# Kernel tuning notes

Hardware: AMD Instinct MI355X
Metric: run time of the kernel (lower is better)

The kernel has to match this reference:

```python
import jax, jax.numpy as jnp
import numpy as np

N_QUBITS = 8


def setup_inputs() -> dict:
    key = jax.random.key(0)
    ks = jax.random.split(key, 6)
    B, S, E, F = 8, 4096, 1024, 4096
    return {
        "x": jax.random.normal(ks[0], (B, S, E), dtype=jnp.float32),
        "theta": jax.random.normal(ks[1], (N_QUBITS,), dtype=jnp.float32),
        "w1": jax.random.normal(ks[2], (F, N_QUBITS), dtype=jnp.float32) * 0.1,
        "b1": jax.random.normal(ks[3], (F,), dtype=jnp.float32) * 0.02,
        "w2": jax.random.normal(ks[4], (E, F), dtype=jnp.float32) * 0.02,
        "b2": jax.random.normal(ks[5], (E,), dtype=jnp.float32) * 0.02,
    }


def reference(x, theta, w1, b1, w2, b2):
    # Quantum layer: per wire i, |0> -RX(x_i)-> -RY(theta_i)-> measure <Z>.
    # No entangling gates => state factorizes; <Z_i> = cos(x_i) * cos(theta_i).
    q = jnp.cos(x[..., :N_QUBITS]) * jnp.cos(theta)  # [B, S, n_qubits]
    h = jax.nn.relu(jnp.einsum("bsq,fq->bsf", q, w1) + b1)  # [B, S, ffn_dim]
    return jnp.einsum("bsf,ef->bse", h, w2) + b2  # [B, S, embed_dim]
```

## Files before the change

kernel.cpp:

```cpp
#include <hip/hip_runtime.h>
#include <stdint.h>

typedef unsigned short u16;
typedef __attribute__((ext_vector_type(8))) short short8v;
typedef __attribute__((ext_vector_type(4))) float float4v;

static __device__ __forceinline__ u16 f2bf(float f) {
    union { float f; uint32_t u; } v; v.f = f;
    uint32_t u = v.u;
    uint32_t r = (u + 0x7fffu + ((u >> 16) & 1u)) >> 16;
    return (u16)r;
}

__global__ __launch_bounds__(256) void w2cvt_kernel(const float* __restrict__ w2,
                                                    u16* __restrict__ W) {
    size_t i = ((size_t)blockIdx.x * 256 + threadIdx.x) * 4;
    float4 v = *(const float4*)&w2[i];
    ushort4 o;
    o.x = f2bf(v.x); o.y = f2bf(v.y); o.z = f2bf(v.z); o.w = f2bf(v.w);
    *(ushort4*)&W[i] = o;
}

__global__ __launch_bounds__(256) void h_kernel(const float* __restrict__ x,
                                                const float* __restrict__ theta,
                                                const float* __restrict__ w1,
                                                const float* __restrict__ b1,
                                                u16* __restrict__ H, int m0) {
    constexpr int ROWS = 16;
    __shared__ float qs[ROWS][8];
    const int tid = threadIdx.x;
    const int r0 = blockIdx.x * ROWS;
    if (tid < ROWS * 8) {
        int r = tid >> 3, i = tid & 7;
        qs[r][i] = cosf(x[(size_t)(m0 + r0 + r) * 1024 + i]) * cosf(theta[i]);
    }
    __syncthreads();
    for (int qi = 0; qi < 4; ++qi) {
        const int f4 = (qi * 256 + tid) * 4;
        float4 wa[4], wb[4];
        float bb[4];
#pragma unroll
        for (int c = 0; c < 4; ++c) {
            wa[c] = *(const float4*)&w1[(size_t)(f4 + c) * 8];
            wb[c] = *(const float4*)&w1[(size_t)(f4 + c) * 8 + 4];
            bb[c] = b1[f4 + c];
        }
        for (int r = 0; r < ROWS; ++r) {
            float qv[8];
#pragma unroll
            for (int i = 0; i < 8; ++i) qv[i] = qs[r][i];
            ushort4 hv;
#pragma unroll
            for (int c = 0; c < 4; ++c) {
                float a = bb[c];
                a += qv[0] * wa[c].x + qv[1] * wa[c].y + qv[2] * wa[c].z + qv[3] * wa[c].w;
                a += qv[4] * wb[c].x + qv[5] * wb[c].y + qv[6] * wb[c].z + qv[7] * wb[c].w;
                a = fmaxf(a, 0.f);
                ((u16*)&hv)[c] = f2bf(a);
            }
            *(ushort4*)&H[(size_t)(r0 + r) * 4096 + f4] = hv;
        }
    }
}

__global__ __launch_bounds__(256) void gemm_kernel(const u16* __restrict__ A,
                                                   const u16* __restrict__ B,
                                                   const float* __restrict__ b2,
                                                   float* __restrict__ C) {
    constexpr int K = 4096, N = 1024;
    constexpr int BM = 128, BK = 64;
    constexpr int NKS = K / BK;
    __shared__ __align__(16) u16 lds[2 * 8192];

    const int tid = threadIdx.x;
    const int wv = tid >> 6, lane = tid & 63;
    const int bn = blockIdx.x & 7, bm = blockIdx.x >> 3;

    auto stage = [&](int ks) {
#pragma unroll
        for (int i = 0; i < 4; ++i) {
            const int sp = wv * 4 + i;
            const int li = sp * 64 + lane;
            const int row = li >> 3;
            const int j = li & 7;
            const int koff = 8 * (j ^ (row & 7));
            const u16* srcA = A + (size_t)(bm * BM + row) * K + ks * BK + koff;
            __builtin_amdgcn_global_load_lds(
                (const __attribute__((address_space(1))) void*)srcA,
                (__attribute__((address_space(3))) void*)&lds[sp * 512], 16, 0, 0);
            const u16* srcB = B + (size_t)(bn * BM + row) * K + ks * BK + koff;
            __builtin_amdgcn_global_load_lds(
                (const __attribute__((address_space(1))) void*)srcB,
                (__attribute__((address_space(3))) void*)&lds[8192 + sp * 512], 16, 0, 0);
        }
    };

    float4v acc[4][4];
#pragma unroll
    for (int mi = 0; mi < 4; ++mi)
#pragma unroll
        for (int ni = 0; ni < 4; ++ni)
            acc[mi][ni] = (float4v){0.f, 0.f, 0.f, 0.f};

    const int wm = (wv & 1) * 64, wn = (wv >> 1) * 64;
    const int lr = lane & 15, kg = lane >> 4;

    stage(0);
    for (int ks = 0; ks < NKS; ++ks) {
        __syncthreads();
#pragma unroll
        for (int kk = 0; kk < 2; ++kk) {
            short8v av[4], bv[4];
#pragma unroll
            for (int mi = 0; mi < 4; ++mi) {
                const int row = wm + mi * 16 + lr;
                const int byteoff = row * 128 + ((kk * 64 + kg * 16) ^ ((row & 7) << 4));
                av[mi] = *(const short8v*)((const char*)lds + byteoff);
            }
#pragma unroll
            for (int ni = 0; ni < 4; ++ni) {
                const int row = wn + ni * 16 + lr;
                const int byteoff = 16384 + row * 128 + ((kk * 64 + kg * 16) ^ ((row & 7) << 4));
                bv[ni] = *(const short8v*)((const char*)lds + byteoff);
            }
#pragma unroll
            for (int mi = 0; mi < 4; ++mi)
#pragma unroll
                for (int ni = 0; ni < 4; ++ni)
                    acc[mi][ni] = __builtin_amdgcn_mfma_f32_16x16x32_bf16(
                        av[mi], bv[ni], acc[mi][ni], 0, 0, 0);
        }
        __syncthreads();
        if (ks + 1 < NKS) stage(ks + 1);
    }

    float b2v[4];
#pragma unroll
    for (int ni = 0; ni < 4; ++ni) b2v[ni] = b2[bn * BM + wn + ni * 16 + lr];
#pragma unroll
    for (int mi = 0; mi < 4; ++mi)
#pragma unroll
        for (int ni = 0; ni < 4; ++ni) {
            const int col = bn * BM + wn + ni * 16 + lr;
#pragma unroll
            for (int j = 0; j < 4; ++j) {
                const int row = bm * BM + wm + mi * 16 + kg * 4 + j;
                C[(size_t)row * N + col] = acc[mi][ni][j] + b2v[ni];
            }
        }
}

__global__ __launch_bounds__(256) void naive_kernel(const float* __restrict__ x,
                                                    const float* __restrict__ theta,
                                                    const float* __restrict__ w1,
                                                    const float* __restrict__ b1,
                                                    const float* __restrict__ w2,
                                                    const float* __restrict__ b2,
                                                    float* __restrict__ out) {
    const int m = blockIdx.x;
    __shared__ float h[4096];
    __shared__ float q[8];
    if (threadIdx.x < 8)
        q[threadIdx.x] = cosf(x[(size_t)m * 1024 + threadIdx.x]) * cosf(theta[threadIdx.x]);
    __syncthreads();
    for (int f = threadIdx.x; f < 4096; f += 256) {
        float a = b1[f];
#pragma unroll
        for (int i = 0; i < 8; ++i) a += q[i] * w1[(size_t)f * 8 + i];
        h[f] = fmaxf(a, 0.f);
    }
    __syncthreads();
    for (int e = threadIdx.x; e < 1024; e += 256) {
        float a = b2[e];
        const float* wr = w2 + (size_t)e * 4096;
        for (int f = 0; f < 4096; ++f) a += h[f] * wr[f];
        out[(size_t)m * 1024 + e] = a;
    }
}

extern "C" void kernel_launch(void* const* d_in, const int* in_sizes, int n_in,
                              void* d_out, int out_size, void* d_ws, size_t ws_size,
                              hipStream_t stream) {
    const float* x     = (const float*)d_in[0];
    const float* theta = (const float*)d_in[1];
    const float* w1    = (const float*)d_in[2];
    const float* b1    = (const float*)d_in[3];
    const float* w2    = (const float*)d_in[4];
    const float* b2    = (const float*)d_in[5];
    float* out = (float*)d_out;

    const int M = 32768, K = 4096, N = 1024;
    const size_t w2b_bytes = (size_t)N * K * 2;

    size_t avail = ws_size > w2b_bytes ? ws_size - w2b_bytes : 0;
    long long mc_ll = (long long)(avail / ((size_t)K * 2));
    int Mc = (int)((mc_ll > 32768) ? 32768 : mc_ll);
    Mc = (Mc / 128) * 128;
    if (Mc > 8192) Mc = 8192;

    if (Mc < 128) {
        naive_kernel<<<dim3(M), dim3(256), 0, stream>>>(x, theta, w1, b1, w2, b2, out);
        return;
    }

    u16* w2b = (u16*)d_ws;
    u16* Hb  = (u16*)((char*)d_ws + w2b_bytes);

    w2cvt_kernel<<<dim3((N * K) / 1024), dim3(256), 0, stream>>>(w2, w2b);

    for (int m0 = 0; m0 < M; m0 += Mc) {
        const int rows = (M - m0 < Mc) ? (M - m0) : Mc;
        h_kernel<<<dim3(rows / 16), dim3(256), 0, stream>>>(x, theta, w1, b1, Hb, m0);
        gemm_kernel<<<dim3((rows / 128) * 8), dim3(256), 0, stream>>>(
            Hb, w2b, b2, out + (size_t)m0 * N);
    }
}
```

Measured before the change: 585.3 us.

## Rework GEMM into 256x128 tile with triple-buffered LDS pipeline and 8 waves

The GEMM moves from 128x128 tiles with 4 waves and a single-stage load to 256x128 tiles with 8 waves. Global-to-LDS loads are triple-buffered two tiles ahead and split across the two k-halves, with explicit vmcnt waits, barriers and setprio around the MFMA blocks, so memory latency overlaps compute. Block indices are remapped so neighbouring blocks share A rows for better L2 reuse. The h_kernel now has each thread write 8 bf16 outputs per row over 32 rows. The cost is larger LDS use (144KB per block) and fragile hand-tuned waitcnt logic.

```diff
diff --git a/kernel.cpp b/kernel.cpp
--- a/kernel.cpp
+++ b/kernel.cpp
@@ -26,74 +26,86 @@
                                                 const float* __restrict__ w1,
                                                 const float* __restrict__ b1,
                                                 u16* __restrict__ H, int m0) {
-    constexpr int ROWS = 16;
-    __shared__ float qs[ROWS][8];
+    __shared__ float qs[32][8];
     const int tid = threadIdx.x;
-    const int r0 = blockIdx.x * ROWS;
-    if (tid < ROWS * 8) {
+    const int rb = blockIdx.x >> 1;
+    const int fb = blockIdx.x & 1;
+    const int r0 = rb * 32;
+    {
         int r = tid >> 3, i = tid & 7;
         qs[r][i] = cosf(x[(size_t)(m0 + r0 + r) * 1024 + i]) * cosf(theta[i]);
     }
     __syncthreads();
-    for (int qi = 0; qi < 4; ++qi) {
-        const int f4 = (qi * 256 + tid) * 4;
-        float4 wa[4], wb[4];
-        float bb[4];
-#pragma unroll
-        for (int c = 0; c < 4; ++c) {
-            wa[c] = *(const float4*)&w1[(size_t)(f4 + c) * 8];
-            wb[c] = *(const float4*)&w1[(size_t)(f4 + c) * 8 + 4];
-            bb[c] = b1[f4 + c];
-        }
-        for (int r = 0; r < ROWS; ++r) {
-            float qv[8];
-#pragma unroll
-            for (int i = 0; i < 8; ++i) qv[i] = qs[r][i];
-            ushort4 hv;
-#pragma unroll
-            for (int c = 0; c < 4; ++c) {
-                float a = bb[c];
-                a += qv[0] * wa[c].x + qv[1] * wa[c].y + qv[2] * wa[c].z + qv[3] * wa[c].w;
-                a += qv[4] * wb[c].x + qv[5] * wb[c].y + qv[6] * wb[c].z + qv[7] * wb[c].w;
-                a = fmaxf(a, 0.f);
-                ((u16*)&hv)[c] = f2bf(a);
-            }
-            *(ushort4*)&H[(size_t)(r0 + r) * 4096 + f4] = hv;
-        }
-    }
-}
-
-__global__ __launch_bounds__(256) void gemm_kernel(const u16* __restrict__ A,
-                                                   const u16* __restrict__ B,
-                                                   const float* __restrict__ b2,
-                                                   float* __restrict__ C) {
+    const int f8 = (fb * 256 + tid) * 8;
+    float4 w[16];
+    float bb[8];
+#pragma unroll
+    for (int c = 0; c < 8; ++c) {
+        w[2 * c]     = *(const float4*)&w1[(size_t)(f8 + c) * 8];
+        w[2 * c + 1] = *(const float4*)&w1[(size_t)(f8 + c) * 8 + 4];
+        bb[c] = b1[f8 + c];
+    }
+    for (int r = 0; r < 32; ++r) {
+        float qv[8];
+#pragma unroll
+        for (int i = 0; i < 8; ++i) qv[i] = qs[r][i];
+        short8v hv;
+#pragma unroll
+        for (int c = 0; c < 8; ++c) {
+            float a = bb[c];
+            a += qv[0] * w[2*c].x + qv[1] * w[2*c].y + qv[2] * w[2*c].z + qv[3] * w[2*c].w;
+            a += qv[4] * w[2*c+1].x + qv[5] * w[2*c+1].y + qv[6] * w[2*c+1].z + qv[7] * w[2*c+1].w;
+            a = fmaxf(a, 0.f);
+            hv[c] = (short)f2bf(a);
+        }
+        *(short8v*)&H[(size_t)(r0 + r) * 4096 + f8] = hv;
+    }
+}
+
+__global__ __launch_bounds__(512, 2) void gemm_kernel(const u16* __restrict__ A,
+                                                      const u16* __restrict__ B,
+                                                      const float* __restrict__ b2,
+                                                      float* __restrict__ C, int nbm) {
     constexpr int K = 4096, N = 1024;
-    constexpr int BM = 128, BK = 64;
-    constexpr int NKS = K / BK;
-    __shared__ __align__(16) u16 lds[2 * 8192];
+    constexpr int NKT = K / 64;
+    __shared__ __align__(16) u16 lds[3 * 24576];
 
     const int tid = threadIdx.x;
     const int wv = tid >> 6, lane = tid & 63;
-    const int bn = blockIdx.x & 7, bm = blockIdx.x >> 3;
-
-    auto stage = [&](int ks) {
-#pragma unroll
-        for (int i = 0; i < 4; ++i) {
-            const int sp = wv * 4 + i;
-            const int li = sp * 64 + lane;
-            const int row = li >> 3;
-            const int j = li & 7;
-            const int koff = 8 * (j ^ (row & 7));
-            const u16* srcA = A + (size_t)(bm * BM + row) * K + ks * BK + koff;
-            __builtin_amdgcn_global_load_lds(
-                (const __attribute__((address_space(1))) void*)srcA,
-                (__attribute__((address_space(3))) void*)&lds[sp * 512], 16, 0, 0);
-            const u16* srcB = B + (size_t)(bn * BM + row) * K + ks * BK + koff;
-            __builtin_amdgcn_global_load_lds(
-                (const __attribute__((address_space(1))) void*)srcB,
-                (__attribute__((address_space(3))) void*)&lds[8192 + sp * 512], 16, 0, 0);
-        }
-    };
+
+    const int qq = nbm;
+    const int bid = (int)blockIdx.x;
+    const int lbid = (bid & 7) * qq + (bid >> 3);
+    const int bm = lbid >> 3, bn = lbid & 7;
+
+    const u16* Ab = A + (size_t)bm * 256 * K;
+    const u16* Bb = B + (size_t)bn * 128 * K;
+
+    const u16* srcA[4]; int dstA[4];
+#pragma unroll
+    for (int u = 0; u < 4; ++u) {
+        const int idx = u * 512 + tid;
+        const int row = idx >> 3, j = idx & 7;
+        srcA[u] = Ab + (size_t)row * K + 8 * (j ^ (row & 7));
+        dstA[u] = idx * 8;
+    }
+    const u16* srcB[2]; int dstB[2];
+#pragma unroll
+    for (int u = 0; u < 2; ++u) {
+        const int idx = u * 512 + tid;
+        const int row = idx >> 3, j = idx & 7;
+        srcB[u] = Bb + (size_t)row * K + 8 * (j ^ (row & 7));
+        dstB[u] = 16384 + idx * 8;
+    }
+
+#define STAGE_A(kt, bufbase, u)                                               \
+    __builtin_amdgcn_global_load_lds(                                         \
+        (const __attribute__((address_space(1))) void*)(srcA[u] + (kt) * 64), \
+        (__attribute__((address_space(3))) void*)((bufbase) + dstA[u]), 16, 0, 0)
+#define STAGE_B(kt, bufbase, u)                                               \
+    __builtin_amdgcn_global_load_lds(                                         \
+        (const __attribute__((address_space(1))) void*)(srcB[u] + (kt) * 64), \
+        (__attribute__((address_space(3))) void*)((bufbase) + dstB[u]), 16, 0, 0)
 
     float4v acc[4][4];
 #pragma unroll
@@ -102,49 +114,91 @@
         for (int ni = 0; ni < 4; ++ni)
             acc[mi][ni] = (float4v){0.f, 0.f, 0.f, 0.f};
 
-    const int wm = (wv & 1) * 64, wn = (wv >> 1) * 64;
+    const int wm = (wv >> 1) * 64, wn = (wv & 1) * 64;
     const int lr = lane & 15, kg = lane >> 4;
 
-    stage(0);
-    for (int ks = 0; ks < NKS; ++ks) {
-        __syncthreads();
-#pragma unroll
-        for (int kk = 0; kk < 2; ++kk) {
-            short8v av[4], bv[4];
-#pragma unroll
-            for (int mi = 0; mi < 4; ++mi) {
-                const int row = wm + mi * 16 + lr;
-                const int byteoff = row * 128 + ((kk * 64 + kg * 16) ^ ((row & 7) << 4));
-                av[mi] = *(const short8v*)((const char*)lds + byteoff);
-            }
-#pragma unroll
-            for (int ni = 0; ni < 4; ++ni) {
-                const int row = wn + ni * 16 + lr;
-                const int byteoff = 16384 + row * 128 + ((kk * 64 + kg * 16) ^ ((row & 7) << 4));
-                bv[ni] = *(const short8v*)((const char*)lds + byteoff);
-            }
-#pragma unroll
-            for (int mi = 0; mi < 4; ++mi)
-#pragma unroll
-                for (int ni = 0; ni < 4; ++ni)
-                    acc[mi][ni] = __builtin_amdgcn_mfma_f32_16x16x32_bf16(
-                        av[mi], bv[ni], acc[mi][ni], 0, 0, 0);
-        }
-        __syncthreads();
-        if (ks + 1 < NKS) stage(ks + 1);
-    }
+    {
+        u16* b0 = &lds[0];
+        u16* b1b = &lds[24576];
+        STAGE_A(0, b0, 0); STAGE_A(0, b0, 1); STAGE_A(0, b0, 2); STAGE_A(0, b0, 3);
+        STAGE_B(0, b0, 0); STAGE_B(0, b0, 1);
+        STAGE_A(1, b1b, 0); STAGE_A(1, b1b, 1); STAGE_A(1, b1b, 2); STAGE_A(1, b1b, 3);
+        STAGE_B(1, b1b, 0); STAGE_B(1, b1b, 1);
+    }
+    asm volatile("s_waitcnt vmcnt(6)" ::: "memory");
+    __builtin_amdgcn_s_barrier();
+
+    int bi = 0, si = 2;
+    for (int kt = 0; kt < NKT; ++kt) {
+        char* buf = (char*)&lds[bi * 24576];
+        u16* sbuf = &lds[si * 24576];
+        const bool doStage = (kt + 2 < NKT);
+
+        if (doStage) { STAGE_A(kt + 2, sbuf, 0); STAGE_A(kt + 2, sbuf, 1); STAGE_A(kt + 2, sbuf, 2); }
+        short8v av0[4], bv0[4];
+#pragma unroll
+        for (int mi = 0; mi < 4; ++mi) {
+            const int row = wm + mi * 16 + lr;
+            av0[mi] = *(const short8v*)(buf + row * 128 + ((kg * 16) ^ ((row & 7) << 4)));
+        }
+#pragma unroll
+        for (int ni = 0; ni < 4; ++ni) {
+            const int row = wn + ni * 16 + lr;
+            bv0[ni] = *(const short8v*)(buf + 32768 + row * 128 + ((kg * 16) ^ ((row & 7) << 4)));
+        }
+        __builtin_amdgcn_s_barrier();
+        __builtin_amdgcn_s_setprio(1);
+#pragma unroll
+        for (int mi = 0; mi < 4; ++mi)
+#pragma unroll
+            for (int ni = 0; ni < 4; ++ni)
+                acc[mi][ni] = __builtin_amdgcn_mfma_f32_16x16x32_bf16(
+                    av0[mi], bv0[ni], acc[mi][ni], 0, 0, 0);
+        __builtin_amdgcn_s_setprio(0);
+        __builtin_amdgcn_s_barrier();
+
+        if (doStage) { STAGE_A(kt + 2, sbuf, 3); STAGE_B(kt + 2, sbuf, 0); STAGE_B(kt + 2, sbuf, 1); }
+        short8v av1[4], bv1[4];
+#pragma unroll
+        for (int mi = 0; mi < 4; ++mi) {
+            const int row = wm + mi * 16 + lr;
+            av1[mi] = *(const short8v*)(buf + row * 128 + ((64 + kg * 16) ^ ((row & 7) << 4)));
+        }
+#pragma unroll
+        for (int ni = 0; ni < 4; ++ni) {
+            const int row = wn + ni * 16 + lr;
+            bv1[ni] = *(const short8v*)(buf + 32768 + row * 128 + ((64 + kg * 16) ^ ((row & 7) << 4)));
+        }
+        if (doStage) asm volatile("s_waitcnt vmcnt(6)" ::: "memory");
+        else         asm volatile("s_waitcnt vmcnt(0)" ::: "memory");
+        __builtin_amdgcn_s_barrier();
+        __builtin_amdgcn_s_setprio(1);
+#pragma unroll
+        for (int mi = 0; mi < 4; ++mi)
+#pragma unroll
+            for (int ni = 0; ni < 4; ++ni)
+                acc[mi][ni] = __builtin_amdgcn_mfma_f32_16x16x32_bf16(
+                    av1[mi], bv1[ni], acc[mi][ni], 0, 0, 0);
+        __builtin_amdgcn_s_setprio(0);
+        __builtin_amdgcn_s_barrier();
+
+        bi = (bi == 2) ? 0 : bi + 1;
+        si = (si == 2) ? 0 : si + 1;
+    }
+#undef STAGE_A
+#undef STAGE_B
 
     float b2v[4];
 #pragma unroll
-    for (int ni = 0; ni < 4; ++ni) b2v[ni] = b2[bn * BM + wn + ni * 16 + lr];
+    for (int ni = 0; ni < 4; ++ni) b2v[ni] = b2[bn * 128 + wn + ni * 16 + lr];
 #pragma unroll
     for (int mi = 0; mi < 4; ++mi)
 #pragma unroll
         for (int ni = 0; ni < 4; ++ni) {
-            const int col = bn * BM + wn + ni * 16 + lr;
+            const int col = bn * 128 + wn + ni * 16 + lr;
 #pragma unroll
             for (int j = 0; j < 4; ++j) {
-                const int row = bm * BM + wm + mi * 16 + kg * 4 + j;
+                const int row = bm * 256 + wm + mi * 16 + kg * 4 + j;
                 C[(size_t)row * N + col] = acc[mi][ni][j] + b2v[ni];
             }
         }
@@ -195,10 +249,10 @@
     size_t avail = ws_size > w2b_bytes ? ws_size - w2b_bytes : 0;
     long long mc_ll = (long long)(avail / ((size_t)K * 2));
     int Mc = (int)((mc_ll > 32768) ? 32768 : mc_ll);
-    Mc = (Mc / 128) * 128;
+    Mc = (Mc / 256) * 256;
     if (Mc > 8192) Mc = 8192;
 
-    if (Mc < 128) {
+    if (Mc < 256) {
         naive_kernel<<<dim3(M), dim3(256), 0, stream>>>(x, theta, w1, b1, w2, b2, out);
         return;
     }
@@ -210,8 +264,8 @@
 
     for (int m0 = 0; m0 < M; m0 += Mc) {
         const int rows = (M - m0 < Mc) ? (M - m0) : Mc;
-        h_kernel<<<dim3(rows / 16), dim3(256), 0, stream>>>(x, theta, w1, b1, Hb, m0);
-        gemm_kernel<<<dim3((rows / 128) * 8), dim3(256), 0, stream>>>(
-            Hb, w2b, b2, out + (size_t)m0 * N);
-    }
-}
+        h_kernel<<<dim3((rows / 32) * 2), dim3(256), 0, stream>>>(x, theta, w1, b1, Hb, m0);
+        const int nbm = rows / 256;
+        gemm_kernel<<<dim3(nbm * 8), dim3(512), 0, stream>>>(Hb, w2b, b2, out + (size_t)m0 * N, nbm);
+    }
+}
```

New measurement: 559.4 us. 1.05x faster.
